# Kernel optimization log

Hardware: AMD Instinct MI355X
Metric: run time of the kernel (lower is better)

The kernel has to match this reference:

```python
import jax, jax.numpy as jnp
import numpy as np

NEG_INF = -1e30  # safe stand-in for -inf (avoids nan in grads, exp underflows to 0)
STOP_IX, CONT_IX = 0, 1


def setup_inputs() -> dict:
    key = jax.random.key(0)
    k1, k2, k3, k4, k5 = jax.random.split(key, 5)
    B, maxT, b, A = 64, 4096, 16, 18
    action_logps = jax.nn.log_softmax(jax.random.normal(k1, (B, maxT + 1, b, A), jnp.float32), axis=-1)
    stop_logps = jax.nn.log_softmax(jax.random.normal(k2, (B, maxT + 1, b, 2), jnp.float32), axis=-1)
    start_logps = jax.nn.log_softmax(jax.random.normal(k3, (B, maxT + 1, b), jnp.float32), axis=-1)
    actions = jax.random.randint(k4, (B, maxT), 0, A, jnp.int32)
    lengths = jax.random.randint(k5, (B,), maxT // 2, maxT + 1, jnp.int32)
    return {"action_logps": action_logps, "stop_logps": stop_logps,
            "start_logps": start_logps, "actions": actions, "lengths": lengths}


def reference(action_logps, stop_logps, start_logps, actions, lengths):
    """Batched, masked HMM forward algorithm.

    action_logps: (B, maxT+1, b, A); stop_logps: (B, maxT+1, b, 2);
    start_logps: (B, maxT+1, b); actions: (B, maxT) int; lengths: (B,) int.
    Returns scalar: -sum_b logp(traj_b).
    """
    B, Tp1, b, A = action_logps.shape
    maxT = Tp1 - 1
    eye = jnp.eye(b, dtype=bool)  # (b, b)

    # f_0 = start_logps[0] + action_logps[0, :, actions[0]]
    al0 = jnp.take_along_axis(action_logps[:, 0], actions[:, 0][:, None, None], axis=2)[..., 0]  # (B, b)
    f0 = start_logps[:, 0] + al0

    def step(f, i):
        beta = stop_logps[:, i, :, STOP_IX]      # (B, b)
        omb = stop_logps[:, i, :, CONT_IX]       # (B, b)
        cont = jnp.where(eye, omb[:, :, None], NEG_INF)                       # (B, b, b) diag
        trans = jnp.logaddexp(beta[:, :, None] + start_logps[:, i, None, :], cont)  # (B, b, b)
        al = jnp.take_along_axis(action_logps[:, i], actions[:, i][:, None, None], axis=2)[..., 0]  # (B, b)
        f_un = f[:, :, None] + trans + al[:, None, :]                          # (B, b, b)
        f_new = jax.scipy.special.logsumexp(f_un, axis=1)                      # (B, b)
        mask = (i < lengths)[:, None]  # original loop runs i = 1..T-1
        return jnp.where(mask, f_new, f), None

    f, _ = jax.lax.scan(step, f0, jnp.arange(1, maxT))

    # total_logp = logsumexp(f + stop_logps[T, :, STOP]) per trajectory
    stop_all = stop_logps[..., STOP_IX]  # (B, Tp1, b)
    stop_T = jnp.take_along_axis(stop_all, lengths[:, None, None].astype(jnp.int32), axis=1)[:, 0]  # (B, b)
    total_logp = jax.scipy.special.logsumexp(f + stop_T, axis=1)  # (B,)
    return -jnp.sum(total_logp)
```

## Files before the change

### kernel.cpp

```cpp
#include <hip/hip_runtime.h>

#define NEGF (-1e30f)

__device__ __forceinline__ float colmax(float v) {
  v = fmaxf(v, __shfl_xor(v, 1));
  v = fmaxf(v, __shfl_xor(v, 2));
  return v;
}
__device__ __forceinline__ float colsum(float v) {
  v += __shfl_xor(v, 1);
  v += __shfl_xor(v, 2);
  return v;
}

struct Step {
  float beta[4], cont[4], es[4], al[4];
};

__device__ __forceinline__ void load_step(
    const float* __restrict__ actl, const float* __restrict__ stopl,
    const float* __restrict__ startl, long bt , int aidx,
    int A, int r, Step& s)
{
  const float4* sp = reinterpret_cast<const float4*>(stopl + bt * 32 + r * 8);
  float4 s0 = sp[0];
  float4 s1 = sp[1];
  s.beta[0] = s0.x; s.cont[0] = s0.y; s.beta[1] = s0.z; s.cont[1] = s0.w;
  s.beta[2] = s1.x; s.cont[2] = s1.y; s.beta[3] = s1.z; s.cont[3] = s1.w;
  float4 st = *reinterpret_cast<const float4*>(startl + bt * 16 + r * 4);
  s.es[0] = __expf(st.x); s.es[1] = __expf(st.y);
  s.es[2] = __expf(st.z); s.es[3] = __expf(st.w);
  const float* ap = actl + bt * (16L * A) + (long)(r * 4) * A + aidx;
  s.al[0] = ap[0];
  s.al[1] = ap[A];
  s.al[2] = ap[2 * A];
  s.al[3] = ap[3 * A];
}

__global__ __launch_bounds__(256) void hmm_chunks(
    const float* __restrict__ action_logps,
    const float* __restrict__ stop_logps,
    const float* __restrict__ start_logps,
    const int* __restrict__ actions,
    const int* __restrict__ lengths,
    float* __restrict__ Mws, float* __restrict__ Offws,
    int B, int maxT, int A, int NC, int CHUNK)
{
  const int lane = threadIdx.x & 63;
  const int gw = blockIdx.x * (blockDim.x >> 6) + (threadIdx.x >> 6);
  if (gw >= B * NC) return;
  const int batch = gw / NC;
  const int chunk = gw % NC;
  const long Tp1 = (long)maxT + 1;
  const int m = lane >> 2;
  const int r = lane & 3;

  float M[4];
#pragma unroll
  for (int q = 0; q < 4; ++q) M[q] = (4 * r + q == m) ? 0.f : NEGF;
  float off = 0.f;

  const int len = lengths[batch];
  const int i0 = 1 + chunk * CHUNK;
  int i1 = i0 + CHUNK;
  if (i1 > maxT) i1 = maxT;
  if (i1 > len) i1 = len;

  if (i0 < i1) {
    const int* actp = actions + (long)batch * maxT;
    const long bt0 = (long)batch * Tp1;
    const int n = i1 - i0;
    Step cur, n1, n2;
    load_step(action_logps, stop_logps, start_logps, bt0 + i0, actp[i0], A, r, cur);
    if (n > 1)
      load_step(action_logps, stop_logps, start_logps, bt0 + i0 + 1, actp[i0 + 1], A, r, n1);
    int a2 = (n > 2) ? actp[i0 + 2] : 0;
    int a3 = (n > 3) ? actp[i0 + 3] : 0;

    for (int i = i0; i < i1; ++i) {
      if (i + 2 < i1)
        load_step(action_logps, stop_logps, start_logps, bt0 + i + 2, a2, A, r, n2);
      a2 = a3;
      a3 = (i + 4 < i1) ? actp[i + 4] : 0;

      float cmax = fmaxf(fmaxf(M[0], M[1]), fmaxf(M[2], M[3]));
      cmax = colmax(cmax);
      float Ms[4];
#pragma unroll
      for (int q = 0; q < 4; ++q) Ms[q] = M[q] - cmax;

      float p = __expf(cur.beta[0] + Ms[0]) + __expf(cur.beta[1] + Ms[1]) +
                __expf(cur.beta[2] + Ms[2]) + __expf(cur.beta[3] + Ms[3]);
      const float ssum = colsum(p);

#pragma unroll
      for (int q = 0; q < 4; ++q) {
        const float e2 = __expf(cur.cont[q] + Ms[q]);
        M[q] = cur.al[q] + __logf(fmaxf(ssum * cur.es[q] + e2, 1e-37f));
      }
      off += cmax;

      cur = n1;
      n1 = n2;
    }
  }

  float4 mv = make_float4(M[0], M[1], M[2], M[3]);
  *reinterpret_cast<float4*>(Mws + (long)gw * 256 + (m * 16 + r * 4)) = mv;
  if (r == 0) Offws[(long)gw * 16 + m] = off;
}

__global__ __launch_bounds__(256) void hmm_combine(
    const float* __restrict__ action_logps,
    const float* __restrict__ stop_logps,
    const float* __restrict__ start_logps,
    const int* __restrict__ actions,
    const int* __restrict__ lengths,
    const float* __restrict__ Mws, const float* __restrict__ Offws,
    float* __restrict__ out,
    int B, int maxT, int A, int NC)
{
  const int batch = blockIdx.x * (blockDim.x >> 6) + (threadIdx.x >> 6);
  if (batch >= B) return;
  const int lane = threadIdx.x & 63;
  const int k = lane & 15;
  const int jg = lane >> 4;
  const long Tp1 = (long)maxT + 1;

  const int a0 = actions[(long)batch * maxT];
  float f = start_logps[(long)batch * Tp1 * 16 + k] +
            action_logps[(long)batch * Tp1 * (16L * A) + (long)k * A + a0];

  const float* Mb = Mws + (long)batch * NC * 256;
  const float* Ob = Offws + (long)batch * NC * 16;

  constexpr int PF = 4;
  float pm[PF][4], po[PF][4];
#pragma unroll
  for (int d = 0; d < PF; ++d) {
#pragma unroll
    for (int q = 0; q < 4; ++q) {
      pm[d][q] = Mb[d * 256 + (4 * jg + q) * 16 + k];
      po[d][q] = Ob[d * 16 + 4 * jg + q];
    }
  }

  for (int cb = 0; cb < NC; cb += PF) {
#pragma unroll
    for (int u = 0; u < PF; ++u) {
      const int c = cb + u;
      float v[4];
      float mx = NEGF;
#pragma unroll
      for (int q = 0; q < 4; ++q) {
        const float fj = __shfl(f, 4 * jg + q);
        v[q] = pm[u][q] + po[u][q] + fj;
        mx = fmaxf(mx, v[q]);
      }
      mx = fmaxf(mx, __shfl_xor(mx, 16));
      mx = fmaxf(mx, __shfl_xor(mx, 32));
      float s = 0.f;
#pragma unroll
      for (int q = 0; q < 4; ++q) s += __expf(v[q] - mx);
      s += __shfl_xor(s, 16);
      s += __shfl_xor(s, 32);
      f = mx + __logf(s);

      const int cn = c + PF;
      if (cn < NC) {
#pragma unroll
        for (int q = 0; q < 4; ++q) {
          pm[u][q] = Mb[(long)cn * 256 + (4 * jg + q) * 16 + k];
          po[u][q] = Ob[cn * 16 + 4 * jg + q];
        }
      }
    }
  }

  const int L = lengths[batch];
  const float st = stop_logps[((long)batch * Tp1 + L) * 32 + k * 2];
  const float v = f + st;
  float mx = v;
  mx = fmaxf(mx, __shfl_xor(mx, 1));
  mx = fmaxf(mx, __shfl_xor(mx, 2));
  mx = fmaxf(mx, __shfl_xor(mx, 4));
  mx = fmaxf(mx, __shfl_xor(mx, 8));
  float s = __expf(v - mx);
  s += __shfl_xor(s, 1);
  s += __shfl_xor(s, 2);
  s += __shfl_xor(s, 4);
  s += __shfl_xor(s, 8);
  const float tot = mx + __logf(s);
  if (lane == 0) atomicAdd(out, -tot);
}

extern "C" void kernel_launch(void* const* d_in, const int* in_sizes, int n_in,
                              void* d_out, int out_size, void* d_ws, size_t ws_size,
                              hipStream_t stream) {
  const float* action_logps = (const float*)d_in[0];
  const float* stop_logps = (const float*)d_in[1];
  const float* start_logps = (const float*)d_in[2];
  const int* actions = (const int*)d_in[3];
  const int* lengths = (const int*)d_in[4];

  const int B = in_sizes[4];
  const int maxT = in_sizes[3] / B;
  const long Tp1 = (long)maxT + 1;
  const int b = (int)((long)in_sizes[1] / ((long)B * Tp1 * 2));
  const int A = (int)((long)in_sizes[0] / ((long)B * Tp1 * b));
  (void)b;

  int NC = 128;
  const size_t per_chunk = (size_t)B * (256 + 16) * sizeof(float);
  if ((size_t)NC * per_chunk > ws_size) {
    NC = (int)(ws_size / per_chunk) & ~3;
    if (NC < 4) NC = 4;
  }
  const int CHUNK = (maxT - 1 + NC - 1) / NC;

  float* Mws = (float*)d_ws;
  float* Offws = Mws + (size_t)B * NC * 256;

  hipMemsetAsync(d_out, 0, (size_t)out_size * sizeof(float), stream);

  const int nwaves = B * NC;
  hmm_chunks<<<dim3((nwaves + 3) / 4), dim3(256), 0, stream>>>(
      action_logps, stop_logps, start_logps, actions, lengths,
      Mws, Offws, B, maxT, A, NC, CHUNK);
  hmm_combine<<<dim3((B + 3) / 4), dim3(256), 0, stream>>>(
      action_logps, stop_logps, start_logps, actions, lengths,
      Mws, Offws, (float*)d_out, B, maxT, A, NC);
}
```

Baseline: 502.6 us.

## Run chunk recurrence in linear probability space with per-lane columns and LDS-staged tiles

The chunk kernel now keeps each of the 16 transfer-matrix columns in one lane as 16 linear-space probabilities. This replaces per-step log/exp with cross-lane shuffles with FMAs plus a per-step max-renormalisation by reciprocal. Each wave handles four chunks. Step parameters are loaded cooperatively one step per lane, exponentiated once, and staged in LDS tiles that are double-buffered against the global loads. The action emission is folded into the next step's coefficients and applied at the end. The cost is more registers per lane and an LDS round-trip, and lanes of one wave share a loop bound set by the first chunk's length.

```diff
diff --git a/kernel.cpp b/kernel.cpp
--- a/kernel.cpp
+++ b/kernel.cpp
@@ -2,112 +2,174 @@
 
 #define NEGF (-1e30f)
 
-__device__ __forceinline__ float colmax(float v) {
-  v = fmaxf(v, __shfl_xor(v, 1));
-  v = fmaxf(v, __shfl_xor(v, 2));
-  return v;
-}
-__device__ __forceinline__ float colsum(float v) {
-  v += __shfl_xor(v, 1);
-  v += __shfl_xor(v, 2);
-  return v;
-}
-
-struct Step {
-  float beta[4], cont[4], es[4], al[4];
-};
-
-__device__ __forceinline__ void load_step(
+constexpr int TILE = 16;
+constexpr int SSTR = 52;
+constexpr int SUBSTR = TILE * SSTR + 4;
+
+__global__ __launch_bounds__(256) void hmm_chunks(
     const float* __restrict__ actl, const float* __restrict__ stopl,
-    const float* __restrict__ startl, long bt , int aidx,
-    int A, int r, Step& s)
+    const float* __restrict__ startl, const int* __restrict__ actions,
+    const int* __restrict__ lengths, float* __restrict__ Mws,
+    float* __restrict__ Offws, int B, int maxT, int A, int NC, int CHUNK)
 {
-  const float4* sp = reinterpret_cast<const float4*>(stopl + bt * 32 + r * 8);
-  float4 s0 = sp[0];
-  float4 s1 = sp[1];
-  s.beta[0] = s0.x; s.cont[0] = s0.y; s.beta[1] = s0.z; s.cont[1] = s0.w;
-  s.beta[2] = s1.x; s.cont[2] = s1.y; s.beta[3] = s1.z; s.cont[3] = s1.w;
-  float4 st = *reinterpret_cast<const float4*>(startl + bt * 16 + r * 4);
-  s.es[0] = __expf(st.x); s.es[1] = __expf(st.y);
-  s.es[2] = __expf(st.z); s.es[3] = __expf(st.w);
-  const float* ap = actl + bt * (16L * A) + (long)(r * 4) * A + aidx;
-  s.al[0] = ap[0];
-  s.al[1] = ap[A];
-  s.al[2] = ap[2 * A];
-  s.al[3] = ap[3 * A];
-}
-
-__global__ __launch_bounds__(256) void hmm_chunks(
-    const float* __restrict__ action_logps,
-    const float* __restrict__ stop_logps,
-    const float* __restrict__ start_logps,
-    const int* __restrict__ actions,
-    const int* __restrict__ lengths,
-    float* __restrict__ Mws, float* __restrict__ Offws,
-    int B, int maxT, int A, int NC, int CHUNK)
-{
+  __shared__ float lds[4 * 4 * SUBSTR];
+  const int wib = threadIdx.x >> 6;
   const int lane = threadIdx.x & 63;
-  const int gw = blockIdx.x * (blockDim.x >> 6) + (threadIdx.x >> 6);
-  if (gw >= B * NC) return;
-  const int batch = gw / NC;
-  const int chunk = gw % NC;
+  const int g = lane >> 4;
+  const int m = lane & 15;
+  const int cpw = NC / 4;
+  const int w = blockIdx.x * 4 + wib;
+  const int batch = w / cpw;
+  if (batch >= B) return;
+  const int chunk = (w % cpw) * 4 + g;
   const long Tp1 = (long)maxT + 1;
-  const int m = lane >> 2;
-  const int r = lane & 3;
-
-  float M[4];
-#pragma unroll
-  for (int q = 0; q < 4; ++q) M[q] = (4 * r + q == m) ? 0.f : NEGF;
-  float off = 0.f;
-
+  const long bt0 = (long)batch * Tp1;
   const int len = lengths[batch];
   const int i0 = 1 + chunk * CHUNK;
-  int i1 = i0 + CHUNK;
-  if (i1 > maxT) i1 = maxT;
-  if (i1 > len) i1 = len;
-
-  if (i0 < i1) {
+  const int cap = min(maxT, len);
+  const int i1 = min(i0 + CHUNK, cap);
+  const int n = max(0, i1 - i0);
+  const int nmax = __shfl(n, 0);
+  float* ldsW = lds + wib * (4 * SUBSTR);
+
+  float P[16];
+#pragma unroll
+  for (int k = 0; k < 16; ++k) P[k] = (k == m) ? 1.f : 0.f;
+  float off = 0.f;
+
+  if (nmax > 0) {
+    const int ntiles = (nmax + TILE - 1) / TILE;
     const int* actp = actions + (long)batch * maxT;
-    const long bt0 = (long)batch * Tp1;
-    const int n = i1 - i0;
-    Step cur, n1, n2;
-    load_step(action_logps, stop_logps, start_logps, bt0 + i0, actp[i0], A, r, cur);
-    if (n > 1)
-      load_step(action_logps, stop_logps, start_logps, bt0 + i0 + 1, actp[i0 + 1], A, r, n1);
-    int a2 = (n > 2) ? actp[i0 + 2] : 0;
-    int a3 = (n > 3) ? actp[i0 + 3] : 0;
-
-    for (int i = i0; i < i1; ++i) {
-      if (i + 2 < i1)
-        load_step(action_logps, stop_logps, start_logps, bt0 + i + 2, a2, A, r, n2);
-      a2 = a3;
-      a3 = (i + 4 < i1) ? actp[i + 4] : 0;
-
-      float cmax = fmaxf(fmaxf(M[0], M[1]), fmaxf(M[2], M[3]));
-      cmax = colmax(cmax);
-      float Ms[4];
-#pragma unroll
-      for (int q = 0; q < 4; ++q) Ms[q] = M[q] - cmax;
-
-      float p = __expf(cur.beta[0] + Ms[0]) + __expf(cur.beta[1] + Ms[1]) +
-                __expf(cur.beta[2] + Ms[2]) + __expf(cur.beta[3] + Ms[3]);
-      const float ssum = colsum(p);
-
+
+    float stv[32], srv[16], alp[16];
+    bool pred = false;
+
+    auto ld = [&](int tile) {
+      const int s = tile * TILE + m;
+      const int i = i0 + s;
+      pred = (s < n);
+      if (pred) {
+        const float4* sv = reinterpret_cast<const float4*>(stopl + (bt0 + i) * 32);
+#pragma unroll
+        for (int q = 0; q < 8; ++q) {
+          float4 v = sv[q];
+          stv[4 * q] = v.x; stv[4 * q + 1] = v.y;
+          stv[4 * q + 2] = v.z; stv[4 * q + 3] = v.w;
+        }
+        const float4* rv = reinterpret_cast<const float4*>(startl + (bt0 + i) * 16);
+#pragma unroll
+        for (int q = 0; q < 4; ++q) {
+          float4 v = rv[q];
+          srv[4 * q] = v.x; srv[4 * q + 1] = v.y;
+          srv[4 * q + 2] = v.z; srv[4 * q + 3] = v.w;
+        }
+        if (s > 0) {
+          const int ap = actp[i - 1];
+          const float* ab = actl + (bt0 + i - 1) * (16L * A) + ap;
+#pragma unroll
+          for (int k = 0; k < 16; ++k) alp[k] = ab[(long)k * A];
+        } else {
+#pragma unroll
+          for (int k = 0; k < 16; ++k) alp[k] = 0.f;
+        }
+      }
+    };
+
+    auto commit = [&]() {
+      float* dst = ldsW + g * SUBSTR + m * SSTR;
+      float ebv[16], cbv[16], esv[16];
+      if (pred) {
+#pragma unroll
+        for (int k = 0; k < 16; ++k) {
+          ebv[k] = __expf(stv[2 * k] + alp[k]);
+          cbv[k] = __expf(stv[2 * k + 1] + alp[k]);
+          esv[k] = __expf(srv[k]);
+        }
+      } else {
+#pragma unroll
+        for (int k = 0; k < 16; ++k) { ebv[k] = 0.f; cbv[k] = 1.f; esv[k] = 0.f; }
+      }
+      float4* d4 = reinterpret_cast<float4*>(dst);
 #pragma unroll
       for (int q = 0; q < 4; ++q) {
-        const float e2 = __expf(cur.cont[q] + Ms[q]);
-        M[q] = cur.al[q] + __logf(fmaxf(ssum * cur.es[q] + e2, 1e-37f));
-      }
-      off += cmax;
-
-      cur = n1;
-      n1 = n2;
+        d4[q] = make_float4(ebv[4 * q], ebv[4 * q + 1], ebv[4 * q + 2], ebv[4 * q + 3]);
+        d4[4 + q] = make_float4(cbv[4 * q], cbv[4 * q + 1], cbv[4 * q + 2], cbv[4 * q + 3]);
+        d4[8 + q] = make_float4(esv[4 * q], esv[4 * q + 1], esv[4 * q + 2], esv[4 * q + 3]);
+      }
+    };
+
+    auto compute_tile = [&]() {
+      const float* src = ldsW + g * SUBSTR;
+#pragma unroll 4
+      for (int ss = 0; ss < TILE; ++ss) {
+        const float4* l4 = reinterpret_cast<const float4*>(src + ss * SSTR);
+        const float4 e0 = l4[0], e1 = l4[1], e2 = l4[2], e3 = l4[3];
+        const float4 c0 = l4[4], c1 = l4[5], c2 = l4[6], c3 = l4[7];
+        const float4 x0 = l4[8], x1 = l4[9], x2 = l4[10], x3 = l4[11];
+        float sb = e0.x * P[0] + e0.y * P[1] + e0.z * P[2] + e0.w * P[3]
+                 + e1.x * P[4] + e1.y * P[5] + e1.z * P[6] + e1.w * P[7]
+                 + e2.x * P[8] + e2.y * P[9] + e2.z * P[10] + e2.w * P[11]
+                 + e3.x * P[12] + e3.y * P[13] + e3.z * P[14] + e3.w * P[15];
+        P[0] = x0.x * sb + c0.x * P[0];   P[1] = x0.y * sb + c0.y * P[1];
+        P[2] = x0.z * sb + c0.z * P[2];   P[3] = x0.w * sb + c0.w * P[3];
+        P[4] = x1.x * sb + c1.x * P[4];   P[5] = x1.y * sb + c1.y * P[5];
+        P[6] = x1.z * sb + c1.z * P[6];   P[7] = x1.w * sb + c1.w * P[7];
+        P[8] = x2.x * sb + c2.x * P[8];   P[9] = x2.y * sb + c2.y * P[9];
+        P[10] = x2.z * sb + c2.z * P[10]; P[11] = x2.w * sb + c2.w * P[11];
+        P[12] = x3.x * sb + c3.x * P[12]; P[13] = x3.y * sb + c3.y * P[13];
+        P[14] = x3.z * sb + c3.z * P[14]; P[15] = x3.w * sb + c3.w * P[15];
+        float c01 = fmaxf(P[0], P[1]),   c23 = fmaxf(P[2], P[3]);
+        float c45 = fmaxf(P[4], P[5]),   c67 = fmaxf(P[6], P[7]);
+        float c89 = fmaxf(P[8], P[9]),   cab = fmaxf(P[10], P[11]);
+        float ccd = fmaxf(P[12], P[13]), cef = fmaxf(P[14], P[15]);
+        float q0 = fmaxf(c01, c23), q1 = fmaxf(c45, c67);
+        float q2 = fmaxf(c89, cab), q3 = fmaxf(ccd, cef);
+        float cmax = fmaxf(fmaxf(q0, q1), fmaxf(q2, q3));
+        cmax = fmaxf(cmax, 1e-30f);
+        const float r = __builtin_amdgcn_rcpf(cmax);
+        off += __logf(cmax);
+#pragma unroll
+        for (int k = 0; k < 16; ++k) P[k] *= r;
+      }
+    };
+
+    ld(0);
+    commit();
+    if (ntiles > 1) ld(1);
+    for (int t = 0; t < ntiles; ++t) {
+      compute_tile();
+      if (t + 1 < ntiles) {
+        commit();
+        if (t + 2 < ntiles) ld(t + 2);
+      }
     }
   }
 
-  float4 mv = make_float4(M[0], M[1], M[2], M[3]);
-  *reinterpret_cast<float4*>(Mws + (long)gw * 256 + (m * 16 + r * 4)) = mv;
-  if (r == 0) Offws[(long)gw * 16 + m] = off;
+  float pal[16];
+  if (n > 0) {
+    const int alast = actions[(long)batch * maxT + (i1 - 1)];
+    const float* ab = actl + (bt0 + i1 - 1) * (16L * A) + alast;
+#pragma unroll
+    for (int k = 0; k < 16; ++k) pal[k] = ab[(long)k * A];
+  } else {
+#pragma unroll
+    for (int k = 0; k < 16; ++k) pal[k] = 0.f;
+  }
+  float o[16];
+#pragma unroll
+  for (int k = 0; k < 16; ++k) {
+    if (n > 0)
+      o[k] = __logf(fmaxf(P[k], 1e-37f)) + pal[k];
+    else
+      o[k] = (k == m) ? 0.f : NEGF;
+  }
+  const long gw = (long)batch * NC + chunk;
+  float4* mv = reinterpret_cast<float4*>(Mws + gw * 256 + m * 16);
+  mv[0] = make_float4(o[0], o[1], o[2], o[3]);
+  mv[1] = make_float4(o[4], o[5], o[6], o[7]);
+  mv[2] = make_float4(o[8], o[9], o[10], o[11]);
+  mv[3] = make_float4(o[12], o[13], o[14], o[15]);
+  Offws[gw * 16 + m] = off;
 }
 
 __global__ __launch_bounds__(256) void hmm_combine(
@@ -223,7 +285,7 @@
 
   hipMemsetAsync(d_out, 0, (size_t)out_size * sizeof(float), stream);
 
-  const int nwaves = B * NC;
+  const int nwaves = B * (NC / 4);
   hmm_chunks<<<dim3((nwaves + 3) / 4), dim3(256), 0, stream>>>(
       action_logps, stop_logps, start_logps, actions, lengths,
       Mws, Offws, B, maxT, A, NC, CHUNK);
```

Result: faster. 474.4 us (-5.6%).
